# Kernel optimization log

Measured on AMD Instinct MI355X. Metric: run time of the kernel, lower is better.

Reference implementation:

```python
import jax, jax.numpy as jnp
import numpy as np

NC = 80          # num classes
NL = 3           # num levels
NA = 3           # anchors per level
MAX_DET = 25     # self.maxdetnum
IOU_THRES = 0.7
MAX_WH = 7680.0  # class offset for class-aware NMS (agnostic=False)


def _xywh2xyxy(b):
    cx, cy, w, h = b[..., 0], b[..., 1], b[..., 2], b[..., 3]
    return jnp.stack((cx - w / 2, cy - h / 2, cx + w / 2, cy + h / 2), -1)


def _decode(xi, anchors_i):
    # xi: (bs, na, ny, nx, nc+5) raw logits -> (bs, na*ny*nx, nc+7)
    bs, na, ny, nx, _ = xi.shape
    y = jax.nn.sigmoid(xi)
    yv, xv = jnp.meshgrid(jnp.arange(ny, dtype=xi.dtype),
                          jnp.arange(nx, dtype=xi.dtype), indexing='ij')
    pos = jnp.stack((xv, yv), -1)                    # (ny, nx, 2): (x_col, y_row) grid coords
    xy = y[..., :2] * 2 + (pos - 0.5)                # grid = pos - 0.5 (as in source: xy*2 + grid)
    wh = (y[..., 2:4] * 2) ** 2 * anchors_i[None, :, None, None, :]
    conf = y[..., 4:]                                # obj + nc class probs
    posb = jnp.broadcast_to(pos, xy.shape)
    out = jnp.concatenate((xy, wh, conf, posb), -1)  # (bs, na, ny, nx, nc+7)
    return out.reshape(bs, -1, out.shape[-1])


def _iou_one_vs_all(box, boxes):
    # xyxy IoU of one box vs (N,4) boxes
    lt = jnp.maximum(box[:2], boxes[:, :2])
    rb = jnp.minimum(box[2:], boxes[:, 2:])
    wh = jnp.clip(rb - lt, 0.0)
    inter = wh[:, 0] * wh[:, 1]
    area1 = (box[2] - box[0]) * (box[3] - box[1])
    area2 = (boxes[:, 2] - boxes[:, 0]) * (boxes[:, 3] - boxes[:, 1])
    return inter / (area1 + area2 - inter)


def _nms_image(pred):
    # pred: (N, nc+7). Note: source computes xc = conf>0.25 but never applies it.
    obj = pred[:, 4]
    cls = pred[:, 5:5 + NC] * obj[:, None]           # x[:,5:-2] *= x[:,4:5]
    box = _xywh2xyxy(pred[:, :4])
    conf = cls.max(axis=1)
    j = jnp.argmax(cls, axis=1).astype(pred.dtype)
    det = jnp.concatenate((box, conf[:, None], j[:, None], pred[:, -2:]), axis=1)  # (N, 8)
    order = jnp.argsort(-conf)                       # score-descending (N < max_nms=30000 so cap is no-op)
    det = det[order]
    boxes = det[:, :4] + det[:, 5:6] * MAX_WH        # class-offset boxes
    n = det.shape[0]

    def body(k, carry):
        valid, sel, selv = carry
        has = valid.any()
        idx = jnp.argmax(valid)                      # first unsuppressed = highest remaining score
        iou = _iou_one_vs_all(boxes[idx], boxes)
        valid = valid & (iou <= IOU_THRES)           # self-IoU = 1 > thres removes idx from pool
        sel = sel.at[k].set(idx)
        selv = selv.at[k].set(has)
        return valid, sel, selv

    valid0 = jnp.ones((n,), bool)
    sel0 = jnp.zeros((MAX_DET,), jnp.int32)
    selv0 = jnp.zeros((MAX_DET,), bool)
    _, sel, selv = jax.lax.fori_loop(0, MAX_DET, body, (valid0, sel0, selv0))
    out = det[sel] * selv[:, None].astype(det.dtype)  # pad invalid slots with zeros
    return out, selv


def _level(feature, xi, anchors_i):
    pred = _decode(xi, anchors_i)                    # (bs, N, nc+7)
    dets, selv = jax.vmap(_nms_image)(pred)          # (bs, MAX_DET, 8), (bs, MAX_DET)
    fmap = jnp.transpose(feature, (0, 2, 3, 1))      # (bs, ny, nx, C)
    row = dets[:, :, 7].astype(jnp.int32)            # det[:, -1] = y grid coord -> posX in source
    col = dets[:, :, 6].astype(jnp.int32)            # det[:, -2] = x grid coord -> posY in source
    gathered = jax.vmap(lambda f, r, c: f[r, c])(fmap, row, col)  # (bs, MAX_DET, C)
    return gathered * selv[:, :, None].astype(fmap.dtype)         # rows beyond n_det stay zero


def setup_inputs() -> dict:
    key = jax.random.key(0)
    ks = jax.random.split(key, 7)
    bs = 16
    grids = [(80, 80), (40, 40), (20, 20)]
    chans = [128, 256, 512]
    inp = {}
    for i, ((ny, nx), c) in enumerate(zip(grids, chans)):
        inp[f"x{i}"] = jax.random.normal(ks[i], (bs, NA, ny, nx, NC + 5), jnp.float32)
        inp[f"features{i}"] = jax.random.normal(ks[3 + i], (bs, c, ny, nx), jnp.float32)
    inp["anchors"] = jax.random.uniform(ks[6], (NL, NA, 2), jnp.float32, 1.0, 6.0)
    return inp


def reference(features0, features1, features2, x0, x1, x2, anchors):
    feats = (features0, features1, features2)
    xs = (x0, x1, x2)
    return tuple(_level(feats[i], xs[i], anchors[i]) for i in range(NL))
```

## Files before the change

kernel.cpp:

```cpp
#include <hip/hip_runtime.h>
#include <math.h>
#include <float.h>

#define MAX_DET 25
#define IOU_THRES 0.7f
#define MAX_WH 7680.0f
#define TOPK 256
#define MCAP 512

__device__ __forceinline__ float sigm(float v) {
#pragma clang fp contract(off)
    return 1.0f / (1.0f + expf(-v));
}

template<int NY, int NX>
__device__ __forceinline__ void decode_body(
    int bid, const float* __restrict__ x, const float* __restrict__ anch,
    float* __restrict__ confW, float* __restrict__ boxW)
{
#pragma clang fp contract(off)
    constexpr int HW = NY * NX;
    constexpr int NPC = 3 * HW;
    int t = bid * 256 + threadIdx.x;
    int g = t >> 2;
    int l4 = t & 3;
    const float* row = x + (long)g * 85;

    float bv = -FLT_MAX; int bc = 0;
#pragma unroll
    for (int j = 0; j < 20; ++j) {
        float v = row[5 + l4 + 4 * j];
        if (v > bv) { bv = v; bc = l4 + 4 * j; }
    }
#pragma unroll
    for (int off = 2; off; off >>= 1) {
        float ov = __shfl_xor(bv, off);
        int   oc = __shfl_xor(bc, off);
        if (ov > bv || (ov == bv && oc < bc)) { bv = ov; bc = oc; }
    }
    if (l4 != 0) return;

    float v0 = row[0], v1 = row[1], v2 = row[2], v3 = row[3], v4 = row[4];
    int i   = g % NPC;
    int a   = i / HW;
    int rem = i - a * HW;
    int gy  = rem / NX;
    int gx  = rem - gy * NX;

    float conf = sigm(bv) * sigm(v4);
    float cx = sigm(v0) * 2.0f + ((float)gx - 0.5f);
    float cy = sigm(v1) * 2.0f + ((float)gy - 0.5f);
    float tw = sigm(v2) * 2.0f, th = sigm(v3) * 2.0f;
    float w = (tw * tw) * anch[a * 2 + 0];
    float h = (th * th) * anch[a * 2 + 1];
    float x1 = cx - w / 2.0f, y1 = cy - h / 2.0f;
    float x2 = cx + w / 2.0f, y2 = cy + h / 2.0f;
    float offc = (float)bc * MAX_WH;

    confW[g] = conf;
    *reinterpret_cast<float4*>(boxW + (long)g * 4) =
        make_float4(x1 + offc, y1 + offc, x2 + offc, y2 + offc);
}

__global__ __launch_bounds__(256) void decode_all_kernel(
    const float* __restrict__ x0, const float* __restrict__ x1, const float* __restrict__ x2,
    const float* __restrict__ anch, float* __restrict__ confW, float* __restrict__ boxW)
{
    int bid = blockIdx.x;
    if (bid < 4800)       decode_body<80, 80>(bid,         x0, anch + 0,  confW,          boxW);
    else if (bid < 6000)  decode_body<40, 40>(bid - 4800,  x1, anch + 6,  confW + 307200, boxW + 307200L * 4);
    else                  decode_body<20, 20>(bid - 6000,  x2, anch + 12, confW + 384000, boxW + 384000L * 4);
}

struct LvlParams {
    const float* feat;
    long candOff;
    long outOff;
    int npc, ny, nx, C;
};

template<int NPC>
__device__ __forceinline__ void run_group(
    const float* __restrict__ gconf, const float* __restrict__ boxW, long base4,
    float* sconf, unsigned long long* sk, unsigned* hist, float (*sbox)[4],
    int* selIdx, int* selValid, unsigned* wtot , unsigned* misc ,
    int grp, int2* __restrict__ sel)
{
#pragma clang fp contract(off)
    const int tid = threadIdx.x;
    const int lane = tid & 63;
    const int wid = tid >> 6;

    const float4* gc4 = (const float4*)gconf;
    float4* sc4 = (float4*)sconf;
    for (int i = tid; i < NPC / 4; i += 1024) sc4[i] = gc4[i];
    if (tid < MAX_DET) selValid[tid] = 0;
    if (tid == 0) misc[0] = 0;

    unsigned B = 0, B2 = 0, K2 = 0;
    for (int pass = 0; pass < 2; ++pass) {
        for (int i = tid; i < 2048; i += 1024) hist[i] = 0;
        __syncthreads();
        for (int i = tid; i < NPC; i += 1024) {
            unsigned bits = __float_as_uint(sconf[i]);
            if (pass == 0) atomicAdd(&hist[bits >> 19], 1u);
            else if ((bits >> 19) == B) atomicAdd(&hist[(bits >> 8) & 2047u], 1u);
        }
        __syncthreads();
        unsigned part = hist[tid * 2] + hist[tid * 2 + 1];
        unsigned s = part;
#pragma unroll
        for (int d = 1; d < 64; d <<= 1) {
            unsigned v = __shfl_down(s, d);
            if (lane < 64 - d) s += v;
        }
        if (lane == 0) wtot[wid] = s;
        __syncthreads();
        unsigned S = s;
        for (int w = wid + 1; w < 16; ++w) S += wtot[w];
        unsigned Ktgt = (pass == 0) ? TOPK : K2;
        if (S >= Ktgt && S - part < Ktgt) {
            unsigned acc = S - part;
            for (int i = 1; i >= 0; --i) {
                unsigned h = hist[tid * 2 + i];
                acc += h;
                if (acc >= Ktgt) { misc[2] = (unsigned)(tid * 2 + i); misc[3] = acc - h; break; }
            }
        }
        __syncthreads();
        if (pass == 0) { B = misc[2]; K2 = Ktgt - misc[3]; }
        else           { B2 = misc[2]; }
        __syncthreads();
    }
    unsigned T = (B << 19) | (B2 << 8);

    for (int i = tid; i < NPC; i += 1024) {
        unsigned bits = __float_as_uint(sconf[i]);
        if (bits >= T) {
            unsigned pos = atomicAdd(&misc[0], 1u);
            if (pos < MCAP)
                sk[pos] = ((unsigned long long)bits << 32) | (unsigned)(~i);
        }
    }
    __syncthreads();
    unsigned cn = misc[0];
    int n = (cn < (unsigned)MCAP) ? (int)cn : MCAP;

    for (int i = tid; i < n; i += 1024) {
        int idx = (int)(~(unsigned)sk[i]);
        const float4 bb4 = *reinterpret_cast<const float4*>(boxW + base4 + (long)idx * 4);
        sbox[i][0] = bb4.x; sbox[i][1] = bb4.y; sbox[i][2] = bb4.z; sbox[i][3] = bb4.w;
    }
    __syncthreads();

    if (tid < 64) {
        unsigned long long kreg[8];
#pragma unroll
        for (int j = 0; j < 8; ++j) {
            int s = tid + 64 * j;
            kreg[j] = (s < n) ? sk[s] : 0ULL;
        }
        float ex1 = 0.f, ey1 = 0.f, ex2 = 0.f, ey2 = 0.f;
        int k = 0;
        while (k < MAX_DET) {
            unsigned long long mk = kreg[0]; int ms = tid;
#pragma unroll
            for (int j = 1; j < 8; ++j)
                if (kreg[j] > mk) { mk = kreg[j]; ms = tid + 64 * j; }
#pragma unroll
            for (int off = 32; off; off >>= 1) {
                unsigned long long ok = __shfl_xor(mk, off);
                int os = __shfl_xor(ms, off);
                if (ok > mk) { mk = ok; ms = os; }
            }
            if (mk == 0ULL) break;
#pragma unroll
            for (int j = 0; j < 8; ++j)
                if (ms == tid + 64 * j) kreg[j] = 0ULL;

            float cx1 = sbox[ms][0], cy1 = sbox[ms][1];
            float cx2 = sbox[ms][2], cy2 = sbox[ms][3];
            bool rej = false;
            if (tid < k) {
                float ltx = fmaxf(ex1, cx1), lty = fmaxf(ey1, cy1);
                float rbx = fminf(ex2, cx2), rby = fminf(ey2, cy2);
                float ww = fmaxf(rbx - ltx, 0.0f), hh = fmaxf(rby - lty, 0.0f);
                float inter = ww * hh;
                float area1 = (ex2 - ex1) * (ey2 - ey1);
                float area2 = (cx2 - cx1) * (cy2 - cy1);
                float iou = inter / (area1 + area2 - inter);
                rej = iou > IOU_THRES;
            }
            rej = __any(rej);
            if (!rej) {
                if (tid == k) { ex1 = cx1; ey1 = cy1; ex2 = cx2; ey2 = cy2; }
                if (tid == 0) { selIdx[k] = (int)(~(unsigned)mk); selValid[k] = 1; }
                ++k;
            }
        }
    }
    __syncthreads();

    if (tid < MAX_DET)
        sel[grp * MAX_DET + tid] = make_int2(selIdx[tid], selValid[tid]);
}

__global__ __launch_bounds__(1024) void select_nms_kernel(
    const float* __restrict__ confW, const float* __restrict__ boxW,
    int2* __restrict__ sel, LvlParams p0, LvlParams p1, LvlParams p2)
{
    __shared__ float sconf[19200];
    __shared__ unsigned long long sk[MCAP];
    __shared__ unsigned hist[2048];
    __shared__ float sbox[MCAP][4];
    __shared__ int   selIdx[MAX_DET];
    __shared__ int   selValid[MAX_DET];
    __shared__ unsigned wtot[16];
    __shared__ unsigned misc[4];

    int grp = blockIdx.x;
    int lvl = grp >> 4, b = grp & 15;
    if (lvl == 0) {
        long base = p0.candOff + (long)b * p0.npc;
        run_group<19200>(confW + base, boxW, base * 4, sconf, sk, hist, sbox, selIdx, selValid, wtot, misc, grp, sel);
    } else if (lvl == 1) {
        long base = p1.candOff + (long)b * p1.npc;
        run_group<4800>(confW + base, boxW, base * 4, sconf, sk, hist, sbox, selIdx, selValid, wtot, misc, grp, sel);
    } else {
        long base = p2.candOff + (long)b * p2.npc;
        run_group<1200>(confW + base, boxW, base * 4, sconf, sk, hist, sbox, selIdx, selValid, wtot, misc, grp, sel);
    }
}

__global__ __launch_bounds__(256) void gather_kernel(
    const int2* __restrict__ sel, float* __restrict__ out,
    LvlParams p0, LvlParams p1, LvlParams p2)
{
    int bid = blockIdx.x;
    int grp = bid / MAX_DET, k = bid - grp * MAX_DET;
    int lvl = grp >> 4, b = grp & 15;
    LvlParams p = (lvl == 0) ? p0 : ((lvl == 1) ? p1 : p2);
    int2 sv = sel[bid];
    long obase = p.outOff + ((long)b * MAX_DET + k) * p.C;
    const int hw = p.ny * p.nx;
    if (sv.y) {
        int rem = sv.x % hw;
        int gy = rem / p.nx, gx = rem - gy * p.nx;
        const float* f = p.feat + (long)b * p.C * hw + (long)gy * p.nx + gx;
        for (int c = threadIdx.x; c < p.C; c += 256)
            out[obase + c] = f[(long)c * hw];
    } else {
        for (int c = threadIdx.x; c < p.C; c += 256)
            out[obase + c] = 0.0f;
    }
}

extern "C" void kernel_launch(void* const* d_in, const int* in_sizes, int n_in,
                              void* d_out, int out_size, void* d_ws, size_t ws_size,
                              hipStream_t stream)
{
    const float* xs[3] = {nullptr, nullptr, nullptr};
    const float* fs[3] = {nullptr, nullptr, nullptr};
    const float* anch  = nullptr;
    for (int i = 0; i < n_in; ++i) {
        const float* p = (const float*)d_in[i];
        switch (in_sizes[i]) {
            case 26112000: xs[0] = p; break;
            case 6528000:  xs[1] = p; break;
            case 1632000:  xs[2] = p; break;
            case 13107200: fs[0] = p; break;
            case 6553600:  fs[1] = p; break;
            case 3276800:  fs[2] = p; break;
            case 18:       anch  = p; break;
        }
    }

    char* wsb = (char*)d_ws;
    float* confW = (float*)wsb;
    float* boxW  = (float*)(wsb + 1612800L);
    int2*  sel   = (int2*)(wsb + 8064000L);

    decode_all_kernel<<<6300, 256, 0, stream>>>(xs[0], xs[1], xs[2], anch, confW, boxW);

    LvlParams P0{fs[0], 0L,      0L,      19200, 80, 80, 128};
    LvlParams P1{fs[1], 307200L, 51200L,  4800,  40, 40, 256};
    LvlParams P2{fs[2], 384000L, 153600L, 1200,  20, 20, 512};

    select_nms_kernel<<<48, 1024, 0, stream>>>(confW, boxW, sel, P0, P1, P2);
    gather_kernel<<<48 * MAX_DET, 256, 0, stream>>>(sel, (float*)d_out, P0, P1, P2);
}
```

Baseline: 63.00 us.

## Decode boxes lazily for top-K candidates and fuse feature gather into NMS

The decode kernel now writes only confidence and a 16-bit best-class index per anchor. Boxes are decoded from the raw logits only for the top-K candidates inside the NMS kernel. The feature gather moves into the NMS kernel, removing the third launch and the intermediate selection buffer, and the histogram is split into two privatized copies to reduce shared atomic contention. This removes the full-size box write and re-read and one kernel launch. In exchange the 48-block NMS kernel takes on strided feature reads and scattered logit reads at low parallelism.

```diff
diff --git a/kernel.cpp b/kernel.cpp
--- a/kernel.cpp
+++ b/kernel.cpp
@@ -13,18 +13,18 @@
     return 1.0f / (1.0f + expf(-v));
 }
 
-template<int NY, int NX>
-__device__ __forceinline__ void decode_body(
-    int bid, const float* __restrict__ x, const float* __restrict__ anch,
-    float* __restrict__ confW, float* __restrict__ boxW)
+__global__ __launch_bounds__(256) void decode_all_kernel(
+    const float* __restrict__ x0, const float* __restrict__ x1, const float* __restrict__ x2,
+    float* __restrict__ confW, unsigned short* __restrict__ bcW)
 {
 #pragma clang fp contract(off)
-    constexpr int HW = NY * NX;
-    constexpr int NPC = 3 * HW;
-    int t = bid * 256 + threadIdx.x;
+    int t = blockIdx.x * 256 + threadIdx.x;
     int g = t >> 2;
     int l4 = t & 3;
-    const float* row = x + (long)g * 85;
+    const float* row;
+    if (g < 307200)       row = x0 + (long)g * 85;
+    else if (g < 384000)  row = x1 + (long)(g - 307200) * 85;
+    else                  row = x2 + (long)(g - 384000) * 85;
 
     float bv = -FLT_MAX; int bc = 0;
 #pragma unroll
@@ -40,53 +40,31 @@
     }
     if (l4 != 0) return;
 
-    float v0 = row[0], v1 = row[1], v2 = row[2], v3 = row[3], v4 = row[4];
-    int i   = g % NPC;
-    int a   = i / HW;
-    int rem = i - a * HW;
-    int gy  = rem / NX;
-    int gx  = rem - gy * NX;
-
-    float conf = sigm(bv) * sigm(v4);
-    float cx = sigm(v0) * 2.0f + ((float)gx - 0.5f);
-    float cy = sigm(v1) * 2.0f + ((float)gy - 0.5f);
-    float tw = sigm(v2) * 2.0f, th = sigm(v3) * 2.0f;
-    float w = (tw * tw) * anch[a * 2 + 0];
-    float h = (th * th) * anch[a * 2 + 1];
-    float x1 = cx - w / 2.0f, y1 = cy - h / 2.0f;
-    float x2 = cx + w / 2.0f, y2 = cy + h / 2.0f;
-    float offc = (float)bc * MAX_WH;
-
-    confW[g] = conf;
-    *reinterpret_cast<float4*>(boxW + (long)g * 4) =
-        make_float4(x1 + offc, y1 + offc, x2 + offc, y2 + offc);
-}
-
-__global__ __launch_bounds__(256) void decode_all_kernel(
-    const float* __restrict__ x0, const float* __restrict__ x1, const float* __restrict__ x2,
-    const float* __restrict__ anch, float* __restrict__ confW, float* __restrict__ boxW)
-{
-    int bid = blockIdx.x;
-    if (bid < 4800)       decode_body<80, 80>(bid,         x0, anch + 0,  confW,          boxW);
-    else if (bid < 6000)  decode_body<40, 40>(bid - 4800,  x1, anch + 6,  confW + 307200, boxW + 307200L * 4);
-    else                  decode_body<20, 20>(bid - 6000,  x2, anch + 12, confW + 384000, boxW + 384000L * 4);
+    float v4 = row[4];
+    confW[g] = sigm(bv) * sigm(v4);
+    bcW[g] = (unsigned short)bc;
 }
 
 struct LvlParams {
     const float* feat;
+    const float* x;
     long candOff;
     long outOff;
-    int npc, ny, nx, C;
+    int C;
 };
 
-template<int NPC>
+template<int NY, int NX>
 __device__ __forceinline__ void run_group(
-    const float* __restrict__ gconf, const float* __restrict__ boxW, long base4,
-    float* sconf, unsigned long long* sk, unsigned* hist, float (*sbox)[4],
+    const float* __restrict__ gconf, const unsigned short* __restrict__ gbc,
+    const float* __restrict__ xg, const float* __restrict__ anch,
+    const float* __restrict__ feat, int C, long outOff, int b,
+    float* sconf, unsigned long long* sk, unsigned* hists, float (*sbox)[4],
     int* selIdx, int* selValid, unsigned* wtot , unsigned* misc ,
-    int grp, int2* __restrict__ sel)
+    float* __restrict__ out)
 {
 #pragma clang fp contract(off)
+    constexpr int HW = NY * NX;
+    constexpr int NPC = 3 * HW;
     const int tid = threadIdx.x;
     const int lane = tid & 63;
     const int wid = tid >> 6;
@@ -99,15 +77,16 @@
 
     unsigned B = 0, B2 = 0, K2 = 0;
     for (int pass = 0; pass < 2; ++pass) {
-        for (int i = tid; i < 2048; i += 1024) hist[i] = 0;
+        for (int i = tid; i < 4096; i += 1024) hists[i] = 0;
         __syncthreads();
         for (int i = tid; i < NPC; i += 1024) {
             unsigned bits = __float_as_uint(sconf[i]);
-            if (pass == 0) atomicAdd(&hist[bits >> 19], 1u);
-            else if ((bits >> 19) == B) atomicAdd(&hist[(bits >> 8) & 2047u], 1u);
-        }
-        __syncthreads();
-        unsigned part = hist[tid * 2] + hist[tid * 2 + 1];
+            if (pass == 0) atomicAdd(&hists[((tid & 1) << 11) + (bits >> 19)], 1u);
+            else if ((bits >> 19) == B) atomicAdd(&hists[((tid & 1) << 11) + ((bits >> 8) & 2047u)], 1u);
+        }
+        __syncthreads();
+        unsigned part = hists[2 * tid] + hists[2 * tid + 1]
+                      + hists[2048 + 2 * tid] + hists[2048 + 2 * tid + 1];
         unsigned s = part;
 #pragma unroll
         for (int d = 1; d < 64; d <<= 1) {
@@ -122,9 +101,10 @@
         if (S >= Ktgt && S - part < Ktgt) {
             unsigned acc = S - part;
             for (int i = 1; i >= 0; --i) {
-                unsigned h = hist[tid * 2 + i];
+                int bin = 2 * tid + i;
+                unsigned h = hists[bin] + hists[2048 + bin];
                 acc += h;
-                if (acc >= Ktgt) { misc[2] = (unsigned)(tid * 2 + i); misc[3] = acc - h; break; }
+                if (acc >= Ktgt) { misc[2] = (unsigned)bin; misc[3] = acc - h; break; }
             }
         }
         __syncthreads();
@@ -148,8 +128,24 @@
 
     for (int i = tid; i < n; i += 1024) {
         int idx = (int)(~(unsigned)sk[i]);
-        const float4 bb4 = *reinterpret_cast<const float4*>(boxW + base4 + (long)idx * 4);
-        sbox[i][0] = bb4.x; sbox[i][1] = bb4.y; sbox[i][2] = bb4.z; sbox[i][3] = bb4.w;
+        const float* row = xg + (long)idx * 85;
+        float v0 = row[0], v1 = row[1], v2 = row[2], v3 = row[3];
+        int bc = (int)gbc[idx];
+        int a   = idx / HW;
+        int rem = idx - a * HW;
+        int gy  = rem / NX;
+        int gx  = rem - gy * NX;
+
+        float cx = sigm(v0) * 2.0f + ((float)gx - 0.5f);
+        float cy = sigm(v1) * 2.0f + ((float)gy - 0.5f);
+        float tw = sigm(v2) * 2.0f, th = sigm(v3) * 2.0f;
+        float w = (tw * tw) * anch[a * 2 + 0];
+        float h = (th * th) * anch[a * 2 + 1];
+        float x1 = cx - w / 2.0f, y1 = cy - h / 2.0f;
+        float x2 = cx + w / 2.0f, y2 = cy + h / 2.0f;
+        float offc = (float)bc * MAX_WH;
+        sbox[i][0] = x1 + offc; sbox[i][1] = y1 + offc;
+        sbox[i][2] = x2 + offc; sbox[i][3] = y2 + offc;
     }
     __syncthreads();
 
@@ -201,17 +197,28 @@
     }
     __syncthreads();
 
-    if (tid < MAX_DET)
-        sel[grp * MAX_DET + tid] = make_int2(selIdx[tid], selValid[tid]);
-}
-
-__global__ __launch_bounds__(1024) void select_nms_kernel(
-    const float* __restrict__ confW, const float* __restrict__ boxW,
-    int2* __restrict__ sel, LvlParams p0, LvlParams p1, LvlParams p2)
+    const float* fb = feat + (long)b * C * HW;
+    long obase = outOff + (long)b * MAX_DET * C;
+    for (int e = tid; e < MAX_DET * C; e += 1024) {
+        int k2 = e / C, c = e - k2 * C;
+        float val = 0.0f;
+        if (selValid[k2]) {
+            int idx = selIdx[k2];
+            int rem = idx % HW;
+            val = fb[(long)c * HW + rem];
+        }
+        out[obase + e] = val;
+    }
+}
+
+__global__ __launch_bounds__(1024) void select_nms_gather_kernel(
+    const float* __restrict__ confW, const unsigned short* __restrict__ bcW,
+    const float* __restrict__ anch, float* __restrict__ out,
+    LvlParams p0, LvlParams p1, LvlParams p2)
 {
     __shared__ float sconf[19200];
     __shared__ unsigned long long sk[MCAP];
-    __shared__ unsigned hist[2048];
+    __shared__ unsigned hists[4096];
     __shared__ float sbox[MCAP][4];
     __shared__ int   selIdx[MAX_DET];
     __shared__ int   selValid[MAX_DET];
@@ -221,37 +228,20 @@
     int grp = blockIdx.x;
     int lvl = grp >> 4, b = grp & 15;
     if (lvl == 0) {
-        long base = p0.candOff + (long)b * p0.npc;
-        run_group<19200>(confW + base, boxW, base * 4, sconf, sk, hist, sbox, selIdx, selValid, wtot, misc, grp, sel);
+        long base = p0.candOff + (long)b * 19200;
+        run_group<80, 80>(confW + base, bcW + base, p0.x + base * 85, anch + 0,
+                          p0.feat, p0.C, p0.outOff, b,
+                          sconf, sk, hists, sbox, selIdx, selValid, wtot, misc, out);
     } else if (lvl == 1) {
-        long base = p1.candOff + (long)b * p1.npc;
-        run_group<4800>(confW + base, boxW, base * 4, sconf, sk, hist, sbox, selIdx, selValid, wtot, misc, grp, sel);
+        long base = p1.candOff + (long)b * 4800;
+        run_group<40, 40>(confW + base, bcW + base, p1.x + (long)b * 4800 * 85, anch + 6,
+                          p1.feat, p1.C, p1.outOff, b,
+                          sconf, sk, hists, sbox, selIdx, selValid, wtot, misc, out);
     } else {
-        long base = p2.candOff + (long)b * p2.npc;
-        run_group<1200>(confW + base, boxW, base * 4, sconf, sk, hist, sbox, selIdx, selValid, wtot, misc, grp, sel);
-    }
-}
-
-__global__ __launch_bounds__(256) void gather_kernel(
-    const int2* __restrict__ sel, float* __restrict__ out,
-    LvlParams p0, LvlParams p1, LvlParams p2)
-{
-    int bid = blockIdx.x;
-    int grp = bid / MAX_DET, k = bid - grp * MAX_DET;
-    int lvl = grp >> 4, b = grp & 15;
-    LvlParams p = (lvl == 0) ? p0 : ((lvl == 1) ? p1 : p2);
-    int2 sv = sel[bid];
-    long obase = p.outOff + ((long)b * MAX_DET + k) * p.C;
-    const int hw = p.ny * p.nx;
-    if (sv.y) {
-        int rem = sv.x % hw;
-        int gy = rem / p.nx, gx = rem - gy * p.nx;
-        const float* f = p.feat + (long)b * p.C * hw + (long)gy * p.nx + gx;
-        for (int c = threadIdx.x; c < p.C; c += 256)
-            out[obase + c] = f[(long)c * hw];
-    } else {
-        for (int c = threadIdx.x; c < p.C; c += 256)
-            out[obase + c] = 0.0f;
+        long base = p2.candOff + (long)b * 1200;
+        run_group<20, 20>(confW + base, bcW + base, p2.x + (long)b * 1200 * 85, anch + 12,
+                          p2.feat, p2.C, p2.outOff, b,
+                          sconf, sk, hists, sbox, selIdx, selValid, wtot, misc, out);
     }
 }
 
@@ -276,16 +266,14 @@
     }
 
     char* wsb = (char*)d_ws;
-    float* confW = (float*)wsb;
-    float* boxW  = (float*)(wsb + 1612800L);
-    int2*  sel   = (int2*)(wsb + 8064000L);
-
-    decode_all_kernel<<<6300, 256, 0, stream>>>(xs[0], xs[1], xs[2], anch, confW, boxW);
-
-    LvlParams P0{fs[0], 0L,      0L,      19200, 80, 80, 128};
-    LvlParams P1{fs[1], 307200L, 51200L,  4800,  40, 40, 256};
-    LvlParams P2{fs[2], 384000L, 153600L, 1200,  20, 20, 512};
-
-    select_nms_kernel<<<48, 1024, 0, stream>>>(confW, boxW, sel, P0, P1, P2);
-    gather_kernel<<<48 * MAX_DET, 256, 0, stream>>>(sel, (float*)d_out, P0, P1, P2);
-}
+    float*          confW = (float*)wsb;
+    unsigned short* bcW   = (unsigned short*)(wsb + 1612800L);
+
+    decode_all_kernel<<<6300, 256, 0, stream>>>(xs[0], xs[1], xs[2], confW, bcW);
+
+    LvlParams P0{fs[0], xs[0] - 0L,        0L,      0L,      128};
+    LvlParams P1{fs[1], xs[1],             307200L, 51200L,  256};
+    LvlParams P2{fs[2], xs[2],             384000L, 153600L, 512};
+
+    select_nms_gather_kernel<<<48, 1024, 0, stream>>>(confW, bcW, anch, (float*)d_out, P0, P1, P2);
+}
```

Result: faster. 61.25 us (-2.8%).
